# Optimization experiments

Measured on AMD Instinct MI355X. Metric: run time of the kernel, lower is better.

The kernel has to match this reference:

```python
import jax, jax.numpy as jnp
import numpy as np

IMG = 64
FS = 96
NH = 6          # num_head == channel dim C (forced by LayerNorm(num_head))
B = 8
HW = IMG * IMG  # 4096
FF = FS * FS    # 9216, Mlp in/hidden features
EPS = 1e-5


def setup_inputs() -> dict:
    key = jax.random.key(0)
    ks = jax.random.split(key, 7)
    x = jax.random.normal(ks[0], (B, NH, HW), jnp.float32)
    feature = jax.random.normal(ks[1], (B, NH, FF), jnp.float32)
    s1 = 1.0 / np.sqrt(FF)
    fc1_w = jax.random.uniform(ks[2], (FF, FF), jnp.float32, -s1, s1)
    fc1_b = jax.random.uniform(ks[3], (FF,), jnp.float32, -s1, s1)
    fc2_w = jax.random.uniform(ks[4], (HW, FF), jnp.float32, -s1, s1)
    fc2_b = jax.random.uniform(ks[5], (HW,), jnp.float32, -s1, s1)
    logit_scale = jnp.log(10.0 * jnp.ones((1, 1, HW), jnp.float32))
    norm_w = jnp.ones((NH,), jnp.float32)
    norm_b = jnp.zeros((NH,), jnp.float32)
    return {"x": x, "feature": feature, "fc1_w": fc1_w, "fc1_b": fc1_b,
            "fc2_w": fc2_w, "fc2_b": fc2_b, "logit_scale": logit_scale,
            "norm_w": norm_w, "norm_b": norm_b}


def reference(x, feature, fc1_w, fc1_b, fc2_w, fc2_b, logit_scale, norm_w, norm_b):
    # x: [B, C, HW]; feature: [B, C, FF]
    xt = jnp.swapaxes(x, 1, 2)                                  # [B, HW, C]
    # Mlp (ReLU act, drop=0): FF -> FF -> HW
    h = jax.nn.relu(jnp.einsum('bcf,hf->bch', feature, fc1_w) + fc1_b)
    f = jnp.einsum('bch,oh->bco', h, fc2_w) + fc2_b             # [B, C, HW]
    # cosine-style logit scale, clamped at log(1/0.01)
    max_log = jnp.log(jnp.float32(100.0))
    ls = jnp.exp(jnp.minimum(logit_scale, max_log))             # [1, 1, HW]
    temp = jnp.einsum('bnc,bcm->bnm', xt, f) * ls               # [B, HW, HW]
    temp = jax.nn.softmax(temp, axis=1)                         # softmax over dim 1
    out = jnp.einsum('bnm,bmc->bnc', temp, xt)                  # [B, HW, C]
    # LayerNorm over last dim (C == num_head), biased variance, eps=1e-5
    mu = jnp.mean(out, axis=-1, keepdims=True)
    var = jnp.mean((out - mu) ** 2, axis=-1, keepdims=True)
    out = (out - mu) / jnp.sqrt(var + EPS) * norm_w + norm_b
    return jnp.swapaxes(out, 1, 2)                              # [B, C, HW]
```

## Files before the change

kernel.cpp:

```cpp
#include <hip/hip_runtime.h>
#include <math.h>

#define BATCH 8
#define CH 6
#define HW 4096
#define FF 9216
#define RC 48
#define LOG2E 1.44269504088896340736f
#define LN100 4.6051701859880913680f

typedef unsigned short u16;
typedef __attribute__((ext_vector_type(4))) float f32x4;
typedef __attribute__((ext_vector_type(8))) short short8;
union F8 { uint4 u; short8 b; };

__device__ __forceinline__ void split1(float f, unsigned& h, unsigned& l) {
    unsigned u = __float_as_uint(f);
    unsigned hb = (u + 0x8000u) & 0xffff0000u;
    h = hb >> 16;
    float r = f - __uint_as_float(hb);
    l = (__float_as_uint(r) + 0x8000u) >> 16;
}

__global__ __launch_bounds__(256) void prep_kernel(
    const float* __restrict__ x, const float* __restrict__ feature,
    u16* __restrict__ fHi, u16* __restrict__ fLo, float* __restrict__ xT)
{
    int i = blockIdx.x * 256 + threadIdx.x;
    if (i < FF * RC) {
        unsigned h, l;
        split1(feature[i], h, l);
        fHi[i] = (u16)h;
        fLo[i] = (u16)l;
    } else {
        int t = i - FF * RC;
        if (t < BATCH * HW * CH) {
            int c = t % CH;
            int n = (t / CH) & (HW - 1);
            int b = t / (HW * CH);
            xT[t] = x[((size_t)(b * CH + c)) * HW + n];
        }
    }
}

__global__ __launch_bounds__(128, 4) void gemm_mfma(
    const float* __restrict__ W, const u16* __restrict__ Ahi,
    const u16* __restrict__ Alo, float* __restrict__ part,
    int N, int kchunk)
{
    const int lane = threadIdx.x & 63;
    const int wv = threadIdx.x >> 6;
    const int col = lane & 15;
    const int kg = lane >> 4;
    const int j0 = blockIdx.x * 64 + wv * 32;
    const int kbase = blockIdx.y * kchunk;
    const int ntiles = kchunk >> 5;

    f32x4 acc[2][3];
#pragma unroll
    for (int jt = 0; jt < 2; ++jt)
#pragma unroll
        for (int mt = 0; mt < 3; ++mt)
            acc[jt][mt] = (f32x4){0.f, 0.f, 0.f, 0.f};

    for (int t = 0; t < ntiles; ++t) {
        const int ko = kbase + t * 32 + kg * 8;
        F8 aH[3], aL[3];
#pragma unroll
        for (int mt = 0; mt < 3; ++mt) {
            size_t off = (size_t)(mt * 16 + col) * FF + ko;
            aH[mt].u = *(const uint4*)(Ahi + off);
            aL[mt].u = *(const uint4*)(Alo + off);
        }
#pragma unroll
        for (int jt = 0; jt < 2; ++jt) {
            const float* wp = W + (size_t)(j0 + jt * 16 + col) * FF + ko;
            float4 w0 = *(const float4*)wp;
            float4 w1 = *(const float4*)(wp + 4);
            float f[8] = {w0.x, w0.y, w0.z, w0.w, w1.x, w1.y, w1.z, w1.w};
            unsigned hh[8], ll[8];
#pragma unroll
            for (int e = 0; e < 8; ++e) split1(f[e], hh[e], ll[e]);
            F8 bH, bL;
            bH.u = make_uint4(hh[0] | (hh[1] << 16), hh[2] | (hh[3] << 16),
                              hh[4] | (hh[5] << 16), hh[6] | (hh[7] << 16));
            bL.u = make_uint4(ll[0] | (ll[1] << 16), ll[2] | (ll[3] << 16),
                              ll[4] | (ll[5] << 16), ll[6] | (ll[7] << 16));
#pragma unroll
            for (int mt = 0; mt < 3; ++mt) {
                acc[jt][mt] = __builtin_amdgcn_mfma_f32_16x16x32_bf16(
                    aH[mt].b, bH.b, acc[jt][mt], 0, 0, 0);
                acc[jt][mt] = __builtin_amdgcn_mfma_f32_16x16x32_bf16(
                    aH[mt].b, bL.b, acc[jt][mt], 0, 0, 0);
                acc[jt][mt] = __builtin_amdgcn_mfma_f32_16x16x32_bf16(
                    aL[mt].b, bH.b, acc[jt][mt], 0, 0, 0);
            }
        }
    }

    const int r0 = (lane >> 4) * 4;
#pragma unroll
    for (int jt = 0; jt < 2; ++jt) {
        int j = j0 + jt * 16 + col;
#pragma unroll
        for (int mt = 0; mt < 3; ++mt) {
            float* dst = part + ((size_t)blockIdx.y * 48 + mt * 16 + r0) * N + j;
#pragma unroll
            for (int q = 0; q < 4; ++q) dst[(size_t)q * N] = acc[jt][mt][q];
        }
    }
}

__global__ __launch_bounds__(256) void reduce_relu(
    const float* __restrict__ part, const float* __restrict__ bias,
    u16* __restrict__ hHi, u16* __restrict__ hLo)
{
    int i = blockIdx.x * 256 + threadIdx.x;
    float s = 0.f;
#pragma unroll
    for (int c = 0; c < 8; ++c) s += part[(size_t)c * (RC * FF) + i];
    int j = i % FF;
    s = fmaxf(s + bias[j], 0.f);
    unsigned h, l;
    split1(s, h, l);
    hHi[i] = (u16)h;
    hLo[i] = (u16)l;
}

__global__ __launch_bounds__(256) void reduce_scale(
    const float* __restrict__ part, const float* __restrict__ bias,
    const float* __restrict__ logit_scale, float* __restrict__ fTs)
{
    int i = blockIdx.x * 256 + threadIdx.x;
    int cc = i % CH;
    int bm = i / CH;
    int m = bm & (HW - 1);
    int b = bm >> 12;
    float s = 0.f;
#pragma unroll
    for (int c = 0; c < 24; ++c)
        s += part[((size_t)c * RC + b * CH + cc) * HW + m];
    float lv = fminf(logit_scale[m], LN100);
    float ls = __builtin_amdgcn_exp2f(lv * LOG2E);
    fTs[i] = (s + bias[m]) * ls * LOG2E;
}

__global__ __launch_bounds__(256) void colsum_kernel(
    const float* __restrict__ fTs, const float* __restrict__ xT,
    float* __restrict__ Dpart)
{
    __shared__ float xs[512 * CH];
    const int t = threadIdx.x;
    const int b = blockIdx.y;
    const int ns = blockIdx.z;
    {
        const float4* src = (const float4*)(xT + ((size_t)b * HW + ns * 512) * CH);
        float4* dst = (float4*)xs;
        dst[t]       = src[t];
        dst[t + 256] = src[t + 256];
        dst[t + 512] = src[t + 512];
    }
    __syncthreads();

    int m = blockIdx.x * 256 + t;
    const float2* f2 = (const float2*)(fTs + ((size_t)b * HW + m) * CH);
    float2 fa = f2[0], fb = f2[1], fc = f2[2];
    float s0 = fa.x, s1 = fa.y, s2 = fb.x, s3 = fb.y, s4 = fc.x, s5 = fc.y;

    float D = 0.f;
#pragma unroll 4
    for (int n = 0; n < 512; ++n) {
        const float* xn = xs + n * CH;
        float a = fmaf(s0, xn[0], fmaf(s1, xn[1], fmaf(s2, xn[2],
                  fmaf(s3, xn[3], fmaf(s4, xn[4], s5 * xn[5])))));
        D += __builtin_amdgcn_exp2f(a);
    }
    Dpart[((size_t)b * 8 + ns) * HW + m] = D;
}

__global__ __launch_bounds__(256) void combineD_kernel(
    const float* __restrict__ Dpart, const float* __restrict__ xT,
    float* __restrict__ xR)
{
    int i = blockIdx.x * 256 + threadIdx.x;
    if (i >= BATCH * HW) return;
    int b = i >> 12, m = i & (HW - 1);
    float s = 0.f;
    for (int ns = 0; ns < 8; ++ns) s += Dpart[((size_t)b * 8 + ns) * HW + m];
    float r = 1.0f / s;
    const float2* xs = (const float2*)(xT + (size_t)i * CH);
    float2 v0 = xs[0], v1 = xs[1], v2 = xs[2];
    float2* xd = (float2*)(xR + (size_t)i * CH);
    xd[0] = make_float2(v0.x * r, v0.y * r);
    xd[1] = make_float2(v1.x * r, v1.y * r);
    xd[2] = make_float2(v2.x * r, v2.y * r);
}

__global__ __launch_bounds__(256) void attn_out_kernel(
    const float* __restrict__ fTs, const float* __restrict__ xT,
    const float* __restrict__ xR, const float* __restrict__ nw,
    const float* __restrict__ nb, float* __restrict__ out)
{
    int b = blockIdx.y;
    int wv = threadIdx.x >> 6;
    int lane = threadIdx.x & 63;
    int n0 = (blockIdx.x * 4 + wv) * 8;

    const float* __restrict__ xb = xT + (size_t)b * HW * CH;
    float xn[8][6];
#pragma unroll
    for (int n = 0; n < 8; ++n)
#pragma unroll
        for (int c = 0; c < 6; ++c) xn[n][c] = xb[(size_t)(n0 + n) * CH + c];

    const float* __restrict__ frb = fTs + (size_t)b * HW * CH;
    const float* __restrict__ xrb = xR + (size_t)b * HW * CH;

    float acc[8][6];
#pragma unroll
    for (int n = 0; n < 8; ++n)
#pragma unroll
        for (int c = 0; c < 6; ++c) acc[n][c] = 0.f;

    for (int i = 0; i < 64; ++i) {
        int m = i * 64 + lane;
        const float2* f2 = (const float2*)(frb + (size_t)m * CH);
        float2 fa = f2[0], fb = f2[1], fc = f2[2];
        const float2* x2 = (const float2*)(xrb + (size_t)m * CH);
        float2 xa = x2[0], xb2 = x2[1], xc = x2[2];
        float f0 = fa.x, f1 = fa.y, f2v = fb.x, f3 = fb.y, f4 = fc.x, f5 = fc.y;
#pragma unroll
        for (int n = 0; n < 8; ++n) {
            float a = fmaf(f0, xn[n][0], fmaf(f1, xn[n][1], fmaf(f2v, xn[n][2],
                      fmaf(f3, xn[n][3], fmaf(f4, xn[n][4], f5 * xn[n][5])))));
            float p = __builtin_amdgcn_exp2f(a);
            acc[n][0] = fmaf(p, xa.x, acc[n][0]);
            acc[n][1] = fmaf(p, xa.y, acc[n][1]);
            acc[n][2] = fmaf(p, xb2.x, acc[n][2]);
            acc[n][3] = fmaf(p, xb2.y, acc[n][3]);
            acc[n][4] = fmaf(p, xc.x, acc[n][4]);
            acc[n][5] = fmaf(p, xc.y, acc[n][5]);
        }
    }

#pragma unroll
    for (int n = 0; n < 8; ++n)
#pragma unroll
        for (int c = 0; c < 6; ++c) {
            float v = acc[n][c];
            for (int d = 1; d < 64; d <<= 1) v += __shfl_xor(v, d, 64);
            acc[n][c] = v;
        }

    if (lane == 0) {
        float wc[6], bc[6];
#pragma unroll
        for (int c = 0; c < 6; ++c) { wc[c] = nw[c]; bc[c] = nb[c]; }
#pragma unroll
        for (int n = 0; n < 8; ++n) {
            float mu = (acc[n][0] + acc[n][1] + acc[n][2] +
                        acc[n][3] + acc[n][4] + acc[n][5]) * (1.f / 6.f);
            float var = 0.f;
#pragma unroll
            for (int c = 0; c < 6; ++c) {
                float dv = acc[n][c] - mu;
                var = fmaf(dv, dv, var);
            }
            var *= (1.f / 6.f);
            float inv = rsqrtf(var + 1e-5f);
#pragma unroll
            for (int c = 0; c < 6; ++c)
                out[((size_t)(b * CH + c)) * HW + n0 + n] =
                    (acc[n][c] - mu) * inv * wc[c] + bc[c];
        }
    }
}

extern "C" void kernel_launch(void* const* d_in, const int* in_sizes, int n_in,
                              void* d_out, int out_size, void* d_ws, size_t ws_size,
                              hipStream_t stream)
{
    const float* x           = (const float*)d_in[0];
    const float* feature     = (const float*)d_in[1];
    const float* fc1_w       = (const float*)d_in[2];
    const float* fc1_b       = (const float*)d_in[3];
    const float* fc2_w       = (const float*)d_in[4];
    const float* fc2_b       = (const float*)d_in[5];
    const float* logit_scale = (const float*)d_in[6];
    const float* norm_w      = (const float*)d_in[7];
    const float* norm_b      = (const float*)d_in[8];
    float* out = (float*)d_out;

    u16* fHi = (u16*)d_ws;
    u16* fLo = fHi + 442368;
    u16* hHi = fLo + 442368;
    u16* hLo = hHi + 442368;
    float* part = (float*)(hLo + 442368);
    float* fTs   = part + 4718592;
    float* xT    = fTs + 196608;
    float* Dpart = xT + 196608;
    float* xR    = Dpart + 262144;

    prep_kernel<<<2496, 256, 0, stream>>>(x, feature, fHi, fLo, xT);
    gemm_mfma<<<dim3(144, 8), 128, 0, stream>>>(fc1_w, fHi, fLo, part, FF, 1152);
    reduce_relu<<<1728, 256, 0, stream>>>(part, fc1_b, hHi, hLo);
    gemm_mfma<<<dim3(64, 24), 128, 0, stream>>>(fc2_w, hHi, hLo, part, HW, 384);
    reduce_scale<<<768, 256, 0, stream>>>(part, fc2_b, logit_scale, fTs);
    colsum_kernel<<<dim3(16, BATCH, 8), 256, 0, stream>>>(fTs, xT, Dpart);
    combineD_kernel<<<(BATCH * HW + 255) / 256, 256, 0, stream>>>(Dpart, xT, xR);
    attn_out_kernel<<<dim3(128, BATCH), 256, 0, stream>>>(fTs, xT, xR, norm_w, norm_b, out);
}
```

Baseline: 730.1 us.

## Deepen split-K for both MLP GEMMs and register-block colsum over four columns

Both MLP GEMMs now split K more finely (16 and 32 chunks instead of 8 and 24), with the reduce kernels summing the extra partials. The launch-bounds occupancy hint drops from 4 to 2, giving the GEMM more registers. The column-sum kernel now has each thread handle four output columns over a 256-row chunk, so each shared-memory x row is reused across four exp computations, and the grid is reshaped to match. The aim is more parallelism in the weight-bandwidth-bound GEMMs and fewer LDS reads per exp, at the cost of more partial-sum traffic and workspace.

Result: no change. 730.9 us (+0.1%).

```diff
diff --git a/kernel.cpp b/kernel.cpp
--- a/kernel.cpp
+++ b/kernel.cpp
@@ -43,7 +43,7 @@
     }
 }
 
-__global__ __launch_bounds__(128, 4) void gemm_mfma(
+__global__ __launch_bounds__(128, 2) void gemm_mfma(
     const float* __restrict__ W, const u16* __restrict__ Ahi,
     const u16* __restrict__ Alo, float* __restrict__ part,
     int N, int kchunk)
@@ -118,7 +118,7 @@
     int i = blockIdx.x * 256 + threadIdx.x;
     float s = 0.f;
 #pragma unroll
-    for (int c = 0; c < 8; ++c) s += part[(size_t)c * (RC * FF) + i];
+    for (int c = 0; c < 16; ++c) s += part[(size_t)c * (RC * FF) + i];
     int j = i % FF;
     s = fmaxf(s + bias[j], 0.f);
     unsigned h, l;
@@ -138,44 +138,55 @@
     int b = bm >> 12;
     float s = 0.f;
 #pragma unroll
-    for (int c = 0; c < 24; ++c)
+    for (int c = 0; c < 32; ++c)
         s += part[((size_t)c * RC + b * CH + cc) * HW + m];
     float lv = fminf(logit_scale[m], LN100);
     float ls = __builtin_amdgcn_exp2f(lv * LOG2E);
     fTs[i] = (s + bias[m]) * ls * LOG2E;
 }
 
+#define NCH 256
 __global__ __launch_bounds__(256) void colsum_kernel(
     const float* __restrict__ fTs, const float* __restrict__ xT,
     float* __restrict__ Dpart)
 {
-    __shared__ float xs[512 * CH];
+    __shared__ float xs[NCH * CH];
     const int t = threadIdx.x;
     const int b = blockIdx.y;
     const int ns = blockIdx.z;
     {
-        const float4* src = (const float4*)(xT + ((size_t)b * HW + ns * 512) * CH);
-        float4* dst = (float4*)xs;
+        const float2* src = (const float2*)(xT + ((size_t)b * HW + ns * NCH) * CH);
+        float2* dst = (float2*)xs;
         dst[t]       = src[t];
         dst[t + 256] = src[t + 256];
         dst[t + 512] = src[t + 512];
     }
     __syncthreads();
 
-    int m = blockIdx.x * 256 + t;
-    const float2* f2 = (const float2*)(fTs + ((size_t)b * HW + m) * CH);
-    float2 fa = f2[0], fb = f2[1], fc = f2[2];
-    float s0 = fa.x, s1 = fa.y, s2 = fb.x, s3 = fb.y, s4 = fc.x, s5 = fc.y;
-
-    float D = 0.f;
-#pragma unroll 4
-    for (int n = 0; n < 512; ++n) {
-        const float* xn = xs + n * CH;
-        float a = fmaf(s0, xn[0], fmaf(s1, xn[1], fmaf(s2, xn[2],
-                  fmaf(s3, xn[3], fmaf(s4, xn[4], s5 * xn[5])))));
-        D += __builtin_amdgcn_exp2f(a);
-    }
-    Dpart[((size_t)b * 8 + ns) * HW + m] = D;
+    const int m0 = blockIdx.x * 1024 + t;
+    float f[4][6];
+#pragma unroll
+    for (int q = 0; q < 4; ++q) {
+        const float2* f2 = (const float2*)(fTs + ((size_t)b * HW + m0 + q * 256) * CH);
+        float2 fa = f2[0], fb = f2[1], fc = f2[2];
+        f[q][0] = fa.x; f[q][1] = fa.y; f[q][2] = fb.x;
+        f[q][3] = fb.y; f[q][4] = fc.x; f[q][5] = fc.y;
+    }
+    float D[4] = {0.f, 0.f, 0.f, 0.f};
+#pragma unroll 2
+    for (int n = 0; n < NCH; ++n) {
+        const float2* xp = (const float2*)(xs + n * CH);
+        float2 x0 = xp[0], x1 = xp[1], x2 = xp[2];
+#pragma unroll
+        for (int q = 0; q < 4; ++q) {
+            float a = fmaf(f[q][0], x0.x, fmaf(f[q][1], x0.y, fmaf(f[q][2], x1.x,
+                      fmaf(f[q][3], x1.y, fmaf(f[q][4], x2.x, f[q][5] * x2.y)))));
+            D[q] += __builtin_amdgcn_exp2f(a);
+        }
+    }
+    float* dp = Dpart + ((size_t)b * 16 + ns) * HW + m0;
+#pragma unroll
+    for (int q = 0; q < 4; ++q) dp[q * 256] = D[q];
 }
 
 __global__ __launch_bounds__(256) void combineD_kernel(
@@ -186,7 +197,8 @@
     if (i >= BATCH * HW) return;
     int b = i >> 12, m = i & (HW - 1);
     float s = 0.f;
-    for (int ns = 0; ns < 8; ++ns) s += Dpart[((size_t)b * 8 + ns) * HW + m];
+#pragma unroll
+    for (int ns = 0; ns < 16; ++ns) s += Dpart[((size_t)b * 16 + ns) * HW + m];
     float r = 1.0f / s;
     const float2* xs = (const float2*)(xT + (size_t)i * CH);
     float2 v0 = xs[0], v1 = xs[1], v2 = xs[2];
@@ -296,17 +308,17 @@
     u16* hHi = fLo + 442368;
     u16* hLo = hHi + 442368;
     float* part = (float*)(hLo + 442368);
-    float* fTs   = part + 4718592;
+    float* fTs   = part + 7077888;
     float* xT    = fTs + 196608;
     float* Dpart = xT + 196608;
-    float* xR    = Dpart + 262144;
+    float* xR    = Dpart + 524288;
 
     prep_kernel<<<2496, 256, 0, stream>>>(x, feature, fHi, fLo, xT);
-    gemm_mfma<<<dim3(144, 8), 128, 0, stream>>>(fc1_w, fHi, fLo, part, FF, 1152);
+    gemm_mfma<<<dim3(144, 16), 128, 0, stream>>>(fc1_w, fHi, fLo, part, FF, 576);
     reduce_relu<<<1728, 256, 0, stream>>>(part, fc1_b, hHi, hLo);
-    gemm_mfma<<<dim3(64, 24), 128, 0, stream>>>(fc2_w, hHi, hLo, part, HW, 384);
+    gemm_mfma<<<dim3(64, 32), 128, 0, stream>>>(fc2_w, hHi, hLo, part, HW, 288);
     reduce_scale<<<768, 256, 0, stream>>>(part, fc2_b, logit_scale, fTs);
-    colsum_kernel<<<dim3(16, BATCH, 8), 256, 0, stream>>>(fTs, xT, Dpart);
+    colsum_kernel<<<dim3(4, BATCH, 16), 256, 0, stream>>>(fTs, xT, Dpart);
     combineD_kernel<<<(BATCH * HW + 255) / 256, 256, 0, stream>>>(Dpart, xT, xR);
     attn_out_kernel<<<dim3(128, BATCH), 256, 0, stream>>>(fTs, xT, xR, norm_w, norm_b, out);
 }
```
